# Kernel tuning notes

Hardware: AMD Instinct MI355X
Metric: run time of the kernel (lower is better)

Reference implementation:

```python
import jax, jax.numpy as jnp
import numpy as np

B, S, OBS, D, H, F, L, A = 64, 512, 128, 512, 8, 2048, 4, 16
KERNEL_EPS = 1e-3  # performer kernel_epsilon
LN_EPS = 1e-6      # flax LayerNorm default


def _layernorm(x, s, b):
    m = jnp.mean(x, axis=-1, keepdims=True)
    v = jnp.mean(jnp.square(x - m), axis=-1, keepdims=True)
    return (x - m) * jax.lax.rsqrt(v + LN_EPS) * s + b


def _favor_attn(x, Wq, bq, Wk, bk, Wv, bv, Wo, bo):
    # FAVOR+ generalized attention, deterministic relu features, bidirectional,
    # renormalize_attention=True. phi(u) = relu(u) + kernel_epsilon.
    Bx, Sx, Dx = x.shape
    hd = Dx // H
    q = (x @ Wq + bq).reshape(Bx, Sx, H, hd)
    k = (x @ Wk + bk).reshape(Bx, Sx, H, hd)
    v = (x @ Wv + bv).reshape(Bx, Sx, H, hd)
    pq = jax.nn.relu(q) + KERNEL_EPS  # [B,S,H,m]
    pk = jax.nn.relu(k) + KERNEL_EPS
    kv = jnp.einsum('bshm,bshd->bhmd', pk, v)      # [B,H,m,hd]
    num = jnp.einsum('bshm,bhmd->bshd', pq, kv)    # [B,S,H,hd]
    ksum = jnp.sum(pk, axis=1)                      # [B,H,m]
    den = jnp.einsum('bshm,bhm->bsh', pq, ksum)    # [B,S,H]
    out = num / den[..., None]
    return out.reshape(Bx, Sx, Dx) @ Wo + bo


def setup_inputs() -> dict:
    key = jax.random.key(0)
    ks = jax.random.split(key, 32)
    sc = lambda *shape: 0.02
    inp = {
        'hidden_state': jax.random.normal(ks[0], (B, 1, D), jnp.float32),
        'ins': jax.random.normal(ks[1], (B, S, OBS), jnp.float32),
        'resets': jax.random.randint(ks[2], (B,), 0, 2) > 0,
        'W_emb': jax.random.normal(ks[3], (OBS, D), jnp.float32) * 0.02,
        'b_emb': jnp.zeros((D,), jnp.float32),
        'Wq': jax.random.normal(ks[4], (L, D, D), jnp.float32) * 0.02,
        'bq': jnp.zeros((L, D), jnp.float32),
        'Wk': jax.random.normal(ks[5], (L, D, D), jnp.float32) * 0.02,
        'bk': jnp.zeros((L, D), jnp.float32),
        'Wv': jax.random.normal(ks[6], (L, D, D), jnp.float32) * 0.02,
        'bv': jnp.zeros((L, D), jnp.float32),
        'Wo': jax.random.normal(ks[7], (L, D, D), jnp.float32) * 0.02,
        'bo': jnp.zeros((L, D), jnp.float32),
        'ln1_s': jnp.ones((L, D), jnp.float32),
        'ln1_b': jnp.zeros((L, D), jnp.float32),
        'ln2_s': jnp.ones((L, D), jnp.float32),
        'ln2_b': jnp.zeros((L, D), jnp.float32),
        'W1': jax.random.normal(ks[8], (L, D, F), jnp.float32) * 0.02,
        'b1': jnp.zeros((L, F), jnp.float32),
        'W2': jax.random.normal(ks[9], (L, F, D), jnp.float32) * 0.02,
        'b2': jnp.zeros((L, D), jnp.float32),
        'W_qp': jax.random.normal(ks[10], (D, A), jnp.float32) * 0.02,
        'b_qp': jnp.zeros((A,), jnp.float32),
    }
    return inp


def reference(hidden_state, ins, resets, W_emb, b_emb, Wq, bq, Wk, bk, Wv, bv,
              Wo, bo, ln1_s, ln1_b, ln2_s, ln2_b, W1, b1, W2, b2, W_qp, b_qp):
    emb = ins @ W_emb + b_emb                                   # [B,S,D]
    h0 = jnp.where(resets[:, None, None], jnp.zeros_like(hidden_state), hidden_state)
    x = jnp.concatenate([h0, emb], axis=1)                      # [B,S+1,D]
    for l in range(Wq.shape[0]):
        att = _favor_attn(x, Wq[l], bq[l], Wk[l], bk[l], Wv[l], bv[l], Wo[l], bo[l])
        x = _layernorm(att + x, ln1_s[l], ln1_b[l])
        ff = jax.nn.relu(x @ W1[l] + b1[l]) @ W2[l] + b2[l]
        x = _layernorm(ff + x, ln2_s[l], ln2_b[l])
    h_out = x[:, 0:1, :]                                        # [B,1,D]
    q_vals = h_out @ W_qp + b_qp                                # [B,1,A]
    return (h_out, q_vals)
```

## Files before the change

kernel.cpp:

```cpp
#include <hip/hip_runtime.h>

typedef __bf16 bf16;
typedef __bf16 bf16x8 __attribute__((ext_vector_type(8)));
typedef float  f32x4  __attribute__((ext_vector_type(4)));


__device__ __forceinline__ void cp16(const bf16* g, bf16* l)
{
    __builtin_amdgcn_global_load_lds(
        (const __attribute__((address_space(1))) void*)g,
        (__attribute__((address_space(3))) void*)l,
        16, 0, 0);
}

__global__ __launch_bounds__(256) void cvt_bf16(
    const float* __restrict__ src, bf16* __restrict__ dst, int n)
{
    for (int i = blockIdx.x * 256 + threadIdx.x; i < n; i += gridDim.x * 256)
        dst[i] = (bf16)src[i];
}

__global__ __launch_bounds__(256) void transpose_f32(
    const float* __restrict__ W, bf16* __restrict__ WT, int K, int N, long elemOff)
{
    __shared__ bf16 tile[32][33];
    const int bn = blockIdx.x * 32;
    const int bk = blockIdx.y * 32;
    const int tx = threadIdx.x & 31, ty = threadIdx.x >> 5;
    for (int r = 0; r < 32; r += 8)
        tile[ty + r][tx] = (bf16)W[elemOff + (long)(bk + ty + r) * N + (bn + tx)];
    __syncthreads();
    for (int r = 0; r < 32; r += 8)
        WT[(long)(bn + ty + r) * K + (bk + tx)] = tile[tx][ty + r];
}

__global__ __launch_bounds__(256) void prep_qkvo(
    const float* __restrict__ Wq, const float* __restrict__ Wk,
    const float* __restrict__ Wv, const float* __restrict__ Wo,
    bf16* __restrict__ WqkvT, bf16* __restrict__ WoT, long elemOff)
{
    __shared__ bf16 tile[32][33];
    const int z = blockIdx.z;
    const float* W = (z == 0) ? Wq : (z == 1) ? Wk : (z == 2) ? Wv : Wo;
    bf16* WT = (z < 3) ? (WqkvT + (long)z * 262144) : WoT;
    const int bn = blockIdx.x * 32;
    const int bk = blockIdx.y * 32;
    const int tx = threadIdx.x & 31, ty = threadIdx.x >> 5;
    for (int r = 0; r < 32; r += 8)
        tile[ty + r][tx] = (bf16)W[elemOff + (long)(bk + ty + r) * 512 + (bn + tx)];
    __syncthreads();
    for (int r = 0; r < 32; r += 8)
        WT[(long)(bn + ty + r) * 512 + (bk + tx)] = tile[tx][ty + r];
}

__global__ __launch_bounds__(256) void prep_ffn(
    const float* __restrict__ W1, const float* __restrict__ W2,
    bf16* __restrict__ W1T, bf16* __restrict__ W2T, long elemOff)
{
    __shared__ bf16 tile[32][33];
    const int z = blockIdx.z;
    const float* W = z ? W2 : W1;
    bf16* WT = z ? W2T : W1T;
    const int N = z ? 512 : 2048;
    const int K = z ? 2048 : 512;
    const int bn = (z ? blockIdx.y : blockIdx.x) * 32;
    const int bk = (z ? blockIdx.x : blockIdx.y) * 32;
    const int tx = threadIdx.x & 31, ty = threadIdx.x >> 5;
    for (int r = 0; r < 32; r += 8)
        tile[ty + r][tx] = (bf16)W[elemOff + (long)(bk + ty + r) * N + (bn + tx)];
    __syncthreads();
    for (int r = 0; r < 32; r += 8)
        WT[(long)(bn + ty + r) * K + (bk + tx)] = tile[tx][ty + r];
}

__global__ __launch_bounds__(256) void concat_all(
    const float* __restrict__ bq, const float* __restrict__ bk,
    const float* __restrict__ bv, float* __restrict__ dst)
{
    const int i = blockIdx.x * 256 + threadIdx.x;
    if (i >= 6144) return;
    const int lay = i / 1536;
    const int rem = i - lay * 1536;
    float v;
    if (rem < 512)        v = bq[lay * 512 + rem];
    else if (rem < 1024)  v = bk[lay * 512 + rem - 512];
    else                  v = bv[lay * 512 + rem - 1024];
    dst[lay * 1536 + rem] = v;
}

__global__ __launch_bounds__(256) void build_x0(
    const float* __restrict__ hs, const int* __restrict__ resets,
    bf16* __restrict__ xb)
{
    const int b = blockIdx.x;
    const bool rz = (resets[b] != 0);
    const long base = (long)b * 513 * 512;
    for (int d = threadIdx.x; d < 512; d += 256)
        xb[base + d] = rz ? (bf16)0.f : (bf16)hs[b * 512 + d];
}

template<int ROWMAP, int ACT, int SCHED>
__global__ __launch_bounds__(256) void gemm128(
    const bf16* __restrict__ A, const bf16* __restrict__ BT,
    const float* __restrict__ bias, bf16* __restrict__ outB,
    int M, int N, int K, int lda, int ldc)
{
    __shared__ bf16 As[(SCHED + 1) * 128 * 32];
    __shared__ bf16 Bs[(SCHED + 1) * 128 * 32];
    const int tid  = threadIdx.x;
    const int wave = tid >> 6;
    const int lane = tid & 63;
    const int q    = lane >> 4;
    const int lm   = lane & 15;
    const int wr   = wave >> 1, wc = wave & 1;

    int flat;
    {
        const int nwg  = gridDim.x * gridDim.y;
        const int orig = blockIdx.y * gridDim.x + blockIdx.x;
        const int qq = nwg >> 3, rr = nwg & 7;
        const int xcd = orig & 7, idx = orig >> 3;
        flat = (xcd < rr ? xcd * (qq + 1) : rr * (qq + 1) + (xcd - rr) * qq) + idx;
    }
    const int bx = flat % gridDim.x;
    const int by = flat / gridDim.x;
    int m0 = by * 128;
    if (m0 > M - 128) m0 = M - 128;
    const int n0 = bx * 128;

    const int r0  = wave * 32 + (lane >> 2);
    const int ksw = ((lane & 3) ^ ((lane >> 2) & 3)) * 8;
    const bf16* Ag0 = A  + (long)(m0 + r0) * lda + ksw;
    const bf16* Ag1 = A  + (long)(m0 + r0 + 16) * lda + ksw;
    const bf16* Bg0 = BT + (long)(n0 + r0) * K + ksw;
    const bf16* Bg1 = BT + (long)(n0 + r0 + 16) * K + ksw;

    const int qx = (q ^ (lm & 3)) * 8;

    f32x4 acc[4][4];
    for (int i = 0; i < 4; i++) for (int j = 0; j < 4; j++)
        for (int r = 0; r < 4; r++) acc[i][j][r] = 0.f;

#define STAGE27(kt, buf)                                       \
    do {                                                       \
        const int _k0 = (kt) * 32;                             \
        cp16(Ag0 + _k0, &As[(buf) * 4096 + wave * 1024]);      \
        cp16(Ag1 + _k0, &As[(buf) * 4096 + wave * 1024 + 512]);\
        cp16(Bg0 + _k0, &Bs[(buf) * 4096 + wave * 1024]);      \
        cp16(Bg1 + _k0, &Bs[(buf) * 4096 + wave * 1024 + 512]);\
    } while (0)
#define COMPUTE27(buf)                                                         \
    do {                                                                       \
        bf16x8 af[4], bfr[4];                                                  \
        _Pragma("unroll")                                                      \
        for (int i = 0; i < 4; i++)                                            \
            af[i] = *(const bf16x8*)(&As[(buf) * 4096 + (wr * 64 + i * 16 + lm) * 32 + qx]); \
        _Pragma("unroll")                                                      \
        for (int j = 0; j < 4; j++)                                            \
            bfr[j] = *(const bf16x8*)(&Bs[(buf) * 4096 + (wc * 64 + j * 16 + lm) * 32 + qx]); \
        _Pragma("unroll")                                                      \
        for (int i = 0; i < 4; i++)                                            \
            _Pragma("unroll")                                                  \
            for (int j = 0; j < 4; j++)                                        \
                acc[i][j] = __builtin_amdgcn_mfma_f32_16x16x32_bf16(           \
                    af[i], bfr[j], acc[i][j], 0, 0, 0);                        \
    } while (0)

    if constexpr (SCHED == 0) {
        for (int k0 = 0; k0 < K; k0 += 32) {
            cp16(Ag0 + k0, &As[wave * 1024]);
            cp16(Ag1 + k0, &As[wave * 1024 + 512]);
            cp16(Bg0 + k0, &Bs[wave * 1024]);
            cp16(Bg1 + k0, &Bs[wave * 1024 + 512]);
            __syncthreads();
            COMPUTE27(0);
            __syncthreads();
        }
    } else if constexpr (SCHED == 1) {
        const int NT = K >> 5;
        STAGE27(0, 0);
        asm volatile("s_waitcnt vmcnt(0)" ::: "memory");
        __builtin_amdgcn_s_barrier();
        int cur = 0;
        for (int t = 0; t < NT; ++t) {
            if (t + 1 < NT) STAGE27(t + 1, cur ^ 1);
            COMPUTE27(cur);
            asm volatile("s_waitcnt vmcnt(0)" ::: "memory");
            __builtin_amdgcn_s_barrier();
            cur ^= 1;
        }
    } else {
        const int NT = K >> 5;
        STAGE27(0, 0);
        STAGE27(1, 1);
        asm volatile("s_waitcnt vmcnt(4)" ::: "memory");
        __builtin_amdgcn_s_barrier();
        int cc = 0, ss = 2;
        for (int t = 0; t < NT; ++t) {
            if (t + 2 < NT) STAGE27(t + 2, ss);
            COMPUTE27(cc);
            if (t + 2 < NT)
                asm volatile("s_waitcnt vmcnt(4)" ::: "memory");
            else
                asm volatile("s_waitcnt vmcnt(0)" ::: "memory");
            __builtin_amdgcn_s_barrier();
            cc = (cc == 2) ? 0 : cc + 1;
            ss = (ss == 2) ? 0 : ss + 1;
        }
    }
#undef COMPUTE27
#undef STAGE27

    #pragma unroll
    for (int j = 0; j < 4; j++) {
        const int col = n0 + wc * 64 + j * 16 + lm;
        const float bv = bias[col];
        #pragma unroll
        for (int i = 0; i < 4; i++) {
            #pragma unroll
            for (int r = 0; r < 4; r++) {
                int row = m0 + wr * 64 + i * 16 + q * 4 + r;
                float vv = acc[i][j][r] + bv;
                if (ACT == 1) vv = fmaxf(vv, 0.f);
                if (ACT == 2) vv = fmaxf(vv, 0.f) + 1e-3f;
                if (ACT == 3 && col < 1024) vv = fmaxf(vv, 0.f) + 1e-3f;
                if (ROWMAP == 1) row = row + (row >> 9) + 1;
                outB[(long)row * ldc + col] = (bf16)vv;
            }
        }
    }
}

#define FP 72
__global__ __launch_bounds__(256) void favor_mfma(bf16* qkv)
{
    const int bh = blockIdx.x;
    const int b = bh >> 3, h = bh & 7;
    const long rbQ = (long)b * 513 * 1536 + h * 64;
    const long rbK = rbQ + 512;
    const long rbV = rbQ + 1024;

    __shared__ bf16 pkT[64][FP];
    __shared__ bf16 vT [64][FP];
    __shared__ bf16 kvT[64][FP];
    __shared__ bf16 pqS[64][FP];
    __shared__ float ksumS[64];
    __shared__ float denS[64];

    const int tid  = threadIdx.x;
    const int wave = tid >> 6;
    const int lane = tid & 63;
    const int q    = lane >> 4;
    const int lm   = lane & 15;
    const int wr   = wave >> 1, wc = wave & 1;

    if (tid < 64) ksumS[tid] = 0.f;

    const int r2   = tid >> 3;
    const int dseg = (tid & 7) * 8;
    const int ra   = 2 * r2;

    float ks8[8];
    #pragma unroll
    for (int e = 0; e < 8; e++) ks8[e] = 0.f;

    f32x4 akv[2][2];
    for (int i = 0; i < 2; i++) for (int j = 0; j < 2; j++)
        for (int r = 0; r < 4; r++) akv[i][j][r] = 0.f;

    for (int t8 = 0; t8 < 9; t8++) {
        const int s0 = t8 * 64;
        const int ga = s0 + ra;
        const int gb = ga + 1;
        bf16x8 pka, pkb, va, vb;
        if (ga < 513) {
            pka = *(const bf16x8*)(qkv + rbK + (long)ga * 1536 + dseg);
            va  = *(const bf16x8*)(qkv + rbV + (long)ga * 1536 + dseg);
        } else {
            #pragma unroll
            for (int e = 0; e < 8; e++) { pka[e] = (bf16)0.f; va[e] = (bf16)0.f; }
        }
        if (gb < 513) {
            pkb = *(const bf16x8*)(qkv + rbK + (long)gb * 1536 + dseg);
            vb  = *(const bf16x8*)(qkv + rbV + (long)gb * 1536 + dseg);
        } else {
            #pragma unroll
            for (int e = 0; e < 8; e++) { pkb[e] = (bf16)0.f; vb[e] = (bf16)0.f; }
        }
        #pragma unroll
        for (int e = 0; e < 8; e++) {
            union { unsigned u; bf16 h[2]; } pw, vw2;
            pw.h[0]  = pka[e]; pw.h[1]  = pkb[e];
            vw2.h[0] = va[e];  vw2.h[1] = vb[e];
            *(unsigned*)&pkT[dseg + e][ra] = pw.u;
            *(unsigned*)&vT [dseg + e][ra] = vw2.u;
            ks8[e] += (float)pka[e] + (float)pkb[e];
        }
        __syncthreads();
        #pragma unroll
        for (int ks = 0; ks < 2; ks++) {
            bf16x8 a0 = *(const bf16x8*)(&pkT[wr * 32 + lm     ][ks * 32 + q * 8]);
            bf16x8 a1 = *(const bf16x8*)(&pkT[wr * 32 + 16 + lm][ks * 32 + q * 8]);
            bf16x8 b0 = *(const bf16x8*)(&vT [wc * 32 + lm     ][ks * 32 + q * 8]);
            bf16x8 b1 = *(const bf16x8*)(&vT [wc * 32 + 16 + lm][ks * 32 + q * 8]);
            akv[0][0] = __builtin_amdgcn_mfma_f32_16x16x32_bf16(a0, b0, akv[0][0], 0, 0, 0);
            akv[0][1] = __builtin_amdgcn_mfma_f32_16x16x32_bf16(a0, b1, akv[0][1], 0, 0, 0);
            akv[1][0] = __builtin_amdgcn_mfma_f32_16x16x32_bf16(a1, b0, akv[1][0], 0, 0, 0);
            akv[1][1] = __builtin_amdgcn_mfma_f32_16x16x32_bf16(a1, b1, akv[1][1], 0, 0, 0);
        }
        __syncthreads();
    }
    #pragma unroll
    for (int e = 0; e < 8; e++)
        atomicAdd(&ksumS[dseg + e], ks8[e]);
    #pragma unroll
    for (int i = 0; i < 2; i++)
        #pragma unroll
        for (int j = 0; j < 2; j++)
            #pragma unroll
            for (int r = 0; r < 4; r++)
                kvT[wc * 32 + j * 16 + lm][wr * 32 + i * 16 + q * 4 + r] =
                    (bf16)akv[i][j][r];
    __syncthreads();

    const int prow = tid >> 2;
    const int pseg = (tid & 3) * 16;
    for (int t8 = 0; t8 < 9; t8++) {
        const int s0 = t8 * 64;
        const int gs = s0 + prow;
        if (gs < 513) {
            *(bf16x8*)(&pqS[prow][pseg])     = *(const bf16x8*)(qkv + rbQ + (long)gs * 1536 + pseg);
            *(bf16x8*)(&pqS[prow][pseg + 8]) = *(const bf16x8*)(qkv + rbQ + (long)gs * 1536 + pseg + 8);
        } else {
            bf16x8 z;
            for (int r = 0; r < 8; r++) z[r] = (bf16)0.f;
            *(bf16x8*)(&pqS[prow][pseg])     = z;
            *(bf16x8*)(&pqS[prow][pseg + 8]) = z;
        }
        __syncthreads();
        {
            const int s = tid >> 2, mb = (tid & 3) * 16;
            float dp = 0.f;
            #pragma unroll
            for (int m2 = 0; m2 < 16; m2++)
                dp += (float)pqS[s][mb + m2] * ksumS[mb + m2];
            dp += __shfl_xor(dp, 1);
            dp += __shfl_xor(dp, 2);
            if ((tid & 3) == 0) denS[s] = dp;
        }
        __syncthreads();
        f32x4 an[4];
        for (int j = 0; j < 4; j++)
            for (int r = 0; r < 4; r++) an[j][r] = 0.f;
        #pragma unroll
        for (int ks = 0; ks < 2; ks++) {
            bf16x8 a = *(const bf16x8*)(&pqS[wave * 16 + lm][ks * 32 + q * 8]);
            #pragma unroll
            for (int j = 0; j < 4; j++) {
                bf16x8 bb = *(const bf16x8*)(&kvT[j * 16 + lm][ks * 32 + q * 8]);
                an[j] = __builtin_amdgcn_mfma_f32_16x16x32_bf16(a, bb, an[j], 0, 0, 0);
            }
        }
        #pragma unroll
        for (int j = 0; j < 4; j++) {
            #pragma unroll
            for (int r = 0; r < 4; r++) {
                const int sl  = wave * 16 + q * 4 + r;
                const int gs2 = s0 + sl;
                if (gs2 < 513) {
                    const int d = j * 16 + lm;
                    qkv[rbQ + (long)gs2 * 1536 + d] = (bf16)(an[j][r] / denS[sl]);
                }
            }
        }
        __syncthreads();
    }
}

__global__ __launch_bounds__(256) void ln_res(
    const bf16* __restrict__ y, int ldy, const float* __restrict__ sc,
    const float* __restrict__ bi, bf16* __restrict__ xb)
{
    const int row  = blockIdx.x * 4 + (threadIdx.x >> 6);
    const int lane = threadIdx.x & 63;
    const bf16* yr = y  + (long)row * ldy + lane * 8;
    bf16*       xr = xb + (long)row * 512 + lane * 8;
    bf16x8 yv = *(const bf16x8*)yr;
    bf16x8 xv = *(const bf16x8*)xr;
    float v[8];
    float sum = 0.f;
    #pragma unroll
    for (int i = 0; i < 8; i++) { v[i] = (float)yv[i] + (float)xv[i]; sum += v[i]; }
    #pragma unroll
    for (int o = 32; o; o >>= 1) sum += __shfl_xor(sum, o);
    const float mean = sum * (1.f / 512.f);
    float vs = 0.f;
    #pragma unroll
    for (int i = 0; i < 8; i++) { float dd = v[i] - mean; vs += dd * dd; }
    #pragma unroll
    for (int o = 32; o; o >>= 1) vs += __shfl_xor(vs, o);
    const float rstd = rsqrtf(vs * (1.f / 512.f) + 1e-6f);
    bf16x8 ov;
    #pragma unroll
    for (int i = 0; i < 8; i++)
        ov[i] = (bf16)((v[i] - mean) * rstd * sc[lane * 8 + i] + bi[lane * 8 + i]);
    *(bf16x8*)xr = ov;
}

__global__ __launch_bounds__(256) void final_head(
    const bf16* __restrict__ xb, const float* __restrict__ Wqp,
    const float* __restrict__ bqp, float* __restrict__ out)
{
    const int b = blockIdx.x;
    const bf16* xr = xb + (long)b * 513 * 512;
    for (int i = threadIdx.x; i < 512; i += 256) out[b * 512 + i] = (float)xr[i];
    const int a = threadIdx.x & 15, g = threadIdx.x >> 4;
    float p = 0.f;
    for (int k = g * 32; k < g * 32 + 32; k++)
        p += (float)xr[k] * Wqp[k * 16 + a];
    __shared__ float red[256];
    red[threadIdx.x] = p;
    __syncthreads();
    if (threadIdx.x < 16) {
        float s = bqp[a];
        for (int g2 = 0; g2 < 16; g2++) s += red[g2 * 16 + a];
        out[64 * 512 + b * 16 + a] = s;
    }
}

extern "C" void kernel_launch(void* const* d_in, const int* in_sizes, int n_in,
                              void* d_out, int out_size, void* d_ws, size_t ws_size,
                              hipStream_t stream)
{
    (void)in_sizes; (void)n_in; (void)out_size; (void)ws_size;
    const float* hs    = (const float*)d_in[0];
    const float* ins   = (const float*)d_in[1];
    const int*   resets= (const int*)d_in[2];
    const float* W_emb = (const float*)d_in[3];
    const float* b_emb = (const float*)d_in[4];
    const float* Wq    = (const float*)d_in[5];
    const float* bq    = (const float*)d_in[6];
    const float* Wk    = (const float*)d_in[7];
    const float* bk    = (const float*)d_in[8];
    const float* Wv    = (const float*)d_in[9];
    const float* bv    = (const float*)d_in[10];
    const float* Wo    = (const float*)d_in[11];
    const float* bo    = (const float*)d_in[12];
    const float* ln1s  = (const float*)d_in[13];
    const float* ln1b  = (const float*)d_in[14];
    const float* ln2s  = (const float*)d_in[15];
    const float* ln2b  = (const float*)d_in[16];
    const float* W1    = (const float*)d_in[17];
    const float* b1    = (const float*)d_in[18];
    const float* W2    = (const float*)d_in[19];
    const float* b2    = (const float*)d_in[20];
    const float* Wqp   = (const float*)d_in[21];
    const float* bqp   = (const float*)d_in[22];
    float* out = (float*)d_out;
    char* ws  = (char*)d_ws;

    bf16* xb   = (bf16*)(ws);
    bf16* qkv  = (bf16*)(ws + 33619968);
    bf16* f    = qkv;
    bf16* y2   = (bf16*)(ws + 33619968 + 67239936);
    bf16* WembT= (bf16*)(ws + 134479872);
    float* bqkv_all = (float*)(ws + 134479872);
    char* LW   = ws + 134610944;
    bf16* WqkvT= (bf16*)(LW + 0);
    bf16* WoT  = (bf16*)(LW + 1572864);
    bf16* W1T  = (bf16*)(LW + 2097152);
    bf16* W2T  = (bf16*)(LW + 4194304);
    bf16* insb = (bf16*)(ws + 140908544);

    cvt_bf16<<<4096, 256, 0, stream>>>(ins, insb, 4194304);
    transpose_f32<<<dim3(16, 4), 256, 0, stream>>>(W_emb, WembT, 128, 512, 0);
    build_x0<<<64, 256, 0, stream>>>(hs, resets, xb);
    gemm128<1, 0, 1><<<dim3(4, 256), 256, 0, stream>>>(
        insb, WembT, b_emb, xb, 32768, 512, 128, 128, 512);
    concat_all<<<24, 256, 0, stream>>>(bq, bk, bv, bqkv_all);

    for (int l = 0; l < 4; l++) {
        const long o512  = (long)l * 262144;
        const long o2048 = (long)l * 1048576;
        prep_qkvo<<<dim3(16, 16, 4), 256, 0, stream>>>(Wq, Wk, Wv, Wo, WqkvT, WoT, o512);
        prep_ffn<<<dim3(64, 16, 2), 256, 0, stream>>>(W1, W2, W1T, W2T, o2048);

        gemm128<0, 3, 0><<<dim3(12, 257), 256, 0, stream>>>(
            xb, WqkvT, bqkv_all + l * 1536, qkv, 32832, 1536, 512, 512, 1536);
        favor_mfma<<<512, 256, 0, stream>>>(qkv);
        gemm128<0, 0, 1><<<dim3(4, 257), 256, 0, stream>>>(
            qkv, WoT, bo + l * 512, qkv + 512, 32832, 512, 512, 1536, 1536);
        ln_res<<<8208, 256, 0, stream>>>(qkv + 512, 1536, ln1s + l * 512, ln1b + l * 512, xb);

        for (int c = 0; c < 2; c++) {
            const long r0 = (long)c * 16416;
            gemm128<0, 1, 0><<<dim3(16, 129), 256, 0, stream>>>(
                xb + r0 * 512, W1T, b1 + l * 2048, f, 16416, 2048, 512, 512, 2048);
            gemm128<0, 0, 2><<<dim3(4, 129), 256, 0, stream>>>(
                f, W2T, b2 + l * 512, y2 + r0 * 512, 16416, 512, 2048, 2048, 512);
        }
        ln_res<<<8208, 256, 0, stream>>>(y2, 512, ln2s + l * 512, ln2b + l * 512, xb);
    }

    final_head<<<64, 256, 0, stream>>>(xb, Wqp, bqp, out);
}
```

Measured before the change: 1.825 ms.

## Use per-wave private LDS double buffering without block barriers in GEMM

Replaces the three-stage shared LDS pipeline with a scheme where each wave stages only its own 64-row slices of A and B into a private LDS region, double-buffered. This removes the block-wide s_barrier from every k-step, relying on per-wave vmcnt/lgkmcnt waits instead. The FFN down-projection launch is switched to the new schedule variant. The cost is duplicated global loads, since waves sharing the same rows or columns each fetch them, plus a larger LDS footprint per block.

```diff
diff --git a/kernel.cpp b/kernel.cpp
--- a/kernel.cpp
+++ b/kernel.cpp
@@ -141,7 +141,7 @@
     for (int i = 0; i < 4; i++) for (int j = 0; j < 4; j++)
         for (int r = 0; r < 4; r++) acc[i][j][r] = 0.f;
 
-#define STAGE27(kt, buf)                                       \
+#define STAGE28(kt, buf)                                       \
     do {                                                       \
         const int _k0 = (kt) * 32;                             \
         cp16(Ag0 + _k0, &As[(buf) * 4096 + wave * 1024]);      \
@@ -149,7 +149,7 @@
         cp16(Bg0 + _k0, &Bs[(buf) * 4096 + wave * 1024]);      \
         cp16(Bg1 + _k0, &Bs[(buf) * 4096 + wave * 1024 + 512]);\
     } while (0)
-#define COMPUTE27(buf)                                                         \
+#define COMPUTE28(buf)                                                         \
     do {                                                                       \
         bf16x8 af[4], bfr[4];                                                  \
         _Pragma("unroll")                                                      \
@@ -173,43 +173,70 @@
             cp16(Bg0 + k0, &Bs[wave * 1024]);
             cp16(Bg1 + k0, &Bs[wave * 1024 + 512]);
             __syncthreads();
-            COMPUTE27(0);
+            COMPUTE28(0);
             __syncthreads();
         }
     } else if constexpr (SCHED == 1) {
         const int NT = K >> 5;
-        STAGE27(0, 0);
+        STAGE28(0, 0);
         asm volatile("s_waitcnt vmcnt(0)" ::: "memory");
         __builtin_amdgcn_s_barrier();
         int cur = 0;
         for (int t = 0; t < NT; ++t) {
-            if (t + 1 < NT) STAGE27(t + 1, cur ^ 1);
-            COMPUTE27(cur);
+            if (t + 1 < NT) STAGE28(t + 1, cur ^ 1);
+            COMPUTE28(cur);
             asm volatile("s_waitcnt vmcnt(0)" ::: "memory");
             __builtin_amdgcn_s_barrier();
             cur ^= 1;
         }
     } else {
         const int NT = K >> 5;
-        STAGE27(0, 0);
-        STAGE27(1, 1);
-        asm volatile("s_waitcnt vmcnt(4)" ::: "memory");
-        __builtin_amdgcn_s_barrier();
-        int cc = 0, ss = 2;
+        const bf16* Agw = A  + (long)(m0 + wr * 64 + (lane >> 2)) * lda + ksw;
+        const bf16* Bgw = BT + (long)(n0 + wc * 64 + (lane >> 2)) * K + ksw;
+        const long lda16 = (long)lda * 16;
+        const long K16   = (long)K * 16;
+        const int  wbase = wave * 4096;
+#define STAGE3(kt, buf)                                            \
+        do {                                                       \
+            const int _k0 = (kt) * 32;                             \
+            const int _d  = wbase + (buf) * 2048;                  \
+            cp16(Agw + _k0,             &As[_d]);                  \
+            cp16(Agw + lda16 + _k0,     &As[_d + 512]);            \
+            cp16(Agw + 2 * lda16 + _k0, &As[_d + 1024]);           \
+            cp16(Agw + 3 * lda16 + _k0, &As[_d + 1536]);           \
+            cp16(Bgw + _k0,             &Bs[_d]);                  \
+            cp16(Bgw + K16 + _k0,       &Bs[_d + 512]);            \
+            cp16(Bgw + 2 * K16 + _k0,   &Bs[_d + 1024]);           \
+            cp16(Bgw + 3 * K16 + _k0,   &Bs[_d + 1536]);           \
+        } while (0)
+        STAGE3(0, 0);
+        STAGE3(1, 1);
         for (int t = 0; t < NT; ++t) {
-            if (t + 2 < NT) STAGE27(t + 2, ss);
-            COMPUTE27(cc);
-            if (t + 2 < NT)
-                asm volatile("s_waitcnt vmcnt(4)" ::: "memory");
+            if (t + 1 < NT)
+                asm volatile("s_waitcnt vmcnt(8)" ::: "memory");
             else
                 asm volatile("s_waitcnt vmcnt(0)" ::: "memory");
-            __builtin_amdgcn_s_barrier();
-            cc = (cc == 2) ? 0 : cc + 1;
-            ss = (ss == 2) ? 0 : ss + 1;
-        }
-    }
-#undef COMPUTE27
-#undef STAGE27
+            const int cb = (t & 1) * 2048 + wbase;
+            bf16x8 af[4], bfr[4];
+            #pragma unroll
+            for (int i = 0; i < 4; i++)
+                af[i] = *(const bf16x8*)(&As[cb + (i * 16 + lm) * 32 + qx]);
+            #pragma unroll
+            for (int j = 0; j < 4; j++)
+                bfr[j] = *(const bf16x8*)(&Bs[cb + (j * 16 + lm) * 32 + qx]);
+            #pragma unroll
+            for (int i = 0; i < 4; i++)
+                #pragma unroll
+                for (int j = 0; j < 4; j++)
+                    acc[i][j] = __builtin_amdgcn_mfma_f32_16x16x32_bf16(
+                        af[i], bfr[j], acc[i][j], 0, 0, 0);
+            asm volatile("s_waitcnt lgkmcnt(0)" ::: "memory");
+            if (t + 2 < NT) STAGE3(t + 2, t & 1);
+        }
+#undef STAGE3
+    }
+#undef COMPUTE28
+#undef STAGE28
 
     #pragma unroll
     for (int j = 0; j < 4; j++) {
@@ -496,7 +523,7 @@
             const long r0 = (long)c * 16416;
             gemm128<0, 1, 0><<<dim3(16, 129), 256, 0, stream>>>(
                 xb + r0 * 512, W1T, b1 + l * 2048, f, 16416, 2048, 512, 512, 2048);
-            gemm128<0, 0, 2><<<dim3(4, 129), 256, 0, stream>>>(
+            gemm128<0, 0, 3><<<dim3(4, 129), 256, 0, stream>>>(
                 f, W2T, b2 + l * 512, y2 + r0 * 512, 16416, 512, 2048, 2048, 512);
         }
         ln_res<<<8208, 256, 0, stream>>>(y2, 512, ln2s + l * 512, ln2b + l * 512, xb);
```

Result: slower. 2.022 ms (+10.8%).
